# Kernel optimization log

Measured on AMD Instinct MI355X. Metric: run time of the kernel, lower is better.

The kernel has to match this reference:

```python
import jax, jax.numpy as jnp
import numpy as np

RATIO = 0.5


def _fps_indices(points, m):
    """Farthest point sampling indices. points: [B,N,3] -> idx [B,m] (int32).
    Deterministic start at index 0 per batch (torch_geometric fps with a fixed start).
    """
    pts = jax.lax.stop_gradient(points)  # index selection is non-differentiable
    B, N, _ = pts.shape
    idx0 = jnp.zeros((B,), dtype=jnp.int32)
    mind0 = jnp.full((B, N), 1e10, dtype=pts.dtype)  # running min sq-distance to selected set

    def step(carry, _):
        mind, last = carry
        last_pt = jnp.take_along_axis(pts, last[:, None, None], axis=1)  # [B,1,3]
        d = jnp.sum((pts - last_pt) ** 2, axis=-1)                       # [B,N]
        mind = jnp.minimum(mind, d)
        nxt = jnp.argmax(mind, axis=1).astype(jnp.int32)                 # farthest point
        return (mind, nxt), nxt

    _, rest = jax.lax.scan(step, (mind0, idx0), None, length=m - 1)      # [m-1, B]
    return jnp.concatenate([idx0[None, :], rest], axis=0).T              # [B, m]


def setup_inputs() -> dict:
    key = jax.random.key(0)
    k1, k2 = jax.random.split(key)
    points = jax.random.normal(k1, (8, 8192, 3), dtype=jnp.float32)
    features = jax.random.normal(k2, (8, 8192, 256), dtype=jnp.float32)
    return {"points": points, "features": features}


def reference(points, features):
    B, N, _ = points.shape
    m = int(np.ceil(RATIO * N))
    idx = _fps_indices(points, m)                                        # [B, m]
    dp = jnp.take_along_axis(points, idx[:, :, None], axis=1)            # [B, m, 3]
    df = jnp.take_along_axis(features, idx[:, :, None], axis=1)          # [B, m, C]
    return dp, df
```

## Files before the change

kernel.cpp:

```cpp
#include <hip/hip_runtime.h>


typedef float v2f __attribute__((ext_vector_type(2)));

#define BATCH 8
#define NPTS  8192
#define MSEL  4096
#define NFEAT 256
#define BLOCK 1024
#define NWAVE (BLOCK / 64)

__device__ __forceinline__ double sqd(double x) {
    double r;
    asm("v_mul_f64 %0, %1, %1" : "=v"(r) : "v"(x));
    return r;
}

__device__ __forceinline__ unsigned wave_umax_rl(unsigned v) {
    unsigned s;
    asm volatile(
        "s_nop 1\n\t"
        "v_max_u32_dpp %1, %1, %1 row_shr:1  row_mask:0xf bank_mask:0xf bound_ctrl:0\n\t"
        "s_nop 1\n\t"
        "v_max_u32_dpp %1, %1, %1 row_shr:2  row_mask:0xf bank_mask:0xf bound_ctrl:0\n\t"
        "s_nop 1\n\t"
        "v_max_u32_dpp %1, %1, %1 row_shr:4  row_mask:0xf bank_mask:0xf bound_ctrl:0\n\t"
        "s_nop 1\n\t"
        "v_max_u32_dpp %1, %1, %1 row_shr:8  row_mask:0xf bank_mask:0xf bound_ctrl:0\n\t"
        "s_nop 1\n\t"
        "v_max_u32_dpp %1, %1, %1 row_bcast:15 row_mask:0xf bank_mask:0xf bound_ctrl:0\n\t"
        "s_nop 1\n\t"
        "v_max_u32_dpp %1, %1, %1 row_bcast:31 row_mask:0xf bank_mask:0xf bound_ctrl:0\n\t"
        "s_nop 1\n\t"
        "v_readlane_b32 %0, %1, 63"
        : "=s"(s), "+v"(v));
    return s;
}

__launch_bounds__(BLOCK, 1)
__global__ void fps_kernel(const float* __restrict__ pts,
                           float* __restrict__ dp,
                           int* __restrict__ idx_out)
{
    __shared__ float s_pts[NPTS * 3];
    __shared__ unsigned long long s_bmax[2];
    __shared__ int s_widx[2];

    const int b    = blockIdx.x;
    const int tid  = threadIdx.x;
    const int lane = tid & 63;
    const float* p = pts + (size_t)b * NPTS * 3;

    for (int i = tid; i < NPTS * 3; i += BLOCK) s_pts[i] = p[i];
    if (tid == 0) {
        s_bmax[0] = 0ull;        s_bmax[1] = 0ull;
        s_widx[0] = 0x7fffffff;  s_widx[1] = 0x7fffffff;
    }

#define DECLP(P, J0, J1) \
    v2f pxp##P = { p[(tid + J0 * 1024) * 3 + 0], p[(tid + J1 * 1024) * 3 + 0] }; \
    v2f pyp##P = { p[(tid + J0 * 1024) * 3 + 1], p[(tid + J1 * 1024) * 3 + 1] }; \
    v2f pzp##P = { p[(tid + J0 * 1024) * 3 + 2], p[(tid + J1 * 1024) * 3 + 2] };
    DECLP(0, 0, 1) DECLP(1, 2, 3) DECLP(2, 4, 5) DECLP(3, 6, 7)
#undef DECLP
    double mind0 = 1e10, mind1 = 1e10, mind2 = 1e10, mind3 = 1e10;
    double mind4 = 1e10, mind5 = 1e10, mind6 = 1e10, mind7 = 1e10;
    float  mfm0 = 1.0001e10f, mfm1 = 1.0001e10f, mfm2 = 1.0001e10f, mfm3 = 1.0001e10f;
    float  mfm4 = 1.0001e10f, mfm5 = 1.0001e10f, mfm6 = 1.0001e10f, mfm7 = 1.0001e10f;

    float cx = p[0], cy = p[1], cz = p[2];
    if (tid == 0) {
        dp[(size_t)b * MSEL * 3 + 0] = cx;
        dp[(size_t)b * MSEL * 3 + 1] = cy;
        dp[(size_t)b * MSEL * 3 + 2] = cz;
        idx_out[b * MSEL + 0] = 0;
    }

    double   tbv   = 0.0;
    bool     dirty = true;
    unsigned whi = 0u, wlo = 0u;
    unsigned wn  = 0x7fffffffu;

    __syncthreads();

    for (int k = 1; k < MSEL; ++k) {
        const v2f cx2 = {cx, cx}, cy2 = {cy, cy}, cz2 = {cz, cz};

#define EX64(PX, PY, PZ, J) { \
        const double ddx = (double)(PX) - (double)cx; \
        const double ddy = (double)(PY) - (double)cy; \
        const double ddz = (double)(PZ) - (double)cz; \
        const double dd  = (sqd(ddx) + sqd(ddy)) + sqd(ddz); \
        if (dd < mind##J) { mind##J = dd; mfm##J = (float)dd * 1.0001f; dirty = true; } }
#define UPDP(P, J0, J1) { \
        const v2f dx = pxp##P - cx2, dy = pyp##P - cy2, dz = pzp##P - cz2; \
        const v2f d  = dx * dx + dy * dy + dz * dz; \
        if (d.x < mfm##J0) EX64(pxp##P.x, pyp##P.x, pzp##P.x, J0) \
        if (d.y < mfm##J1) EX64(pxp##P.y, pyp##P.y, pzp##P.y, J1) }
        UPDP(0, 0, 1) UPDP(1, 2, 3) UPDP(2, 4, 5) UPDP(3, 6, 7)
#undef UPDP
#undef EX64

        if (__any(dirty)) {
            const double a0 = fmax(mind0, mind1), a1 = fmax(mind2, mind3);
            const double a2 = fmax(mind4, mind5), a3 = fmax(mind6, mind7);
            tbv = fmax(fmax(a0, a1), fmax(a2, a3));
            dirty = false;

            const unsigned long long tb = (unsigned long long)__double_as_longlong(tbv);
            const unsigned thi = (unsigned)(tb >> 32);
            const unsigned tlo = (unsigned)tb;
            whi = wave_umax_rl(thi);
            wlo = wave_umax_rl(thi == whi ? tlo : 0u);

            int n = 0x7fffffff;
            if (thi == whi && tlo == wlo) {
                if (mind7 == tbv) n = tid + 7 * 1024;
                if (mind6 == tbv) n = tid + 6 * 1024;
                if (mind5 == tbv) n = tid + 5 * 1024;
                if (mind4 == tbv) n = tid + 4 * 1024;
                if (mind3 == tbv) n = tid + 3 * 1024;
                if (mind2 == tbv) n = tid + 2 * 1024;
                if (mind1 == tbv) n = tid + 1 * 1024;
                if (mind0 == tbv) n = tid;
            }
            wn = ~wave_umax_rl(~(unsigned)n);
        }

        const unsigned long long mybits =
            ((unsigned long long)whi << 32) | (unsigned long long)wlo;
        if (lane == 0) atomicMax(&s_bmax[k & 1], mybits);
        __syncthreads();

        const unsigned long long bmaxbits = s_bmax[k & 1];
        if (tid == 0) {
            s_bmax[(k + 1) & 1] = 0ull;
            s_widx[(k + 1) & 1] = 0x7fffffff;
        }

        if (lane == 0 && mybits == bmaxbits)
            atomicMin(&s_widx[k & 1], (int)wn);
        __syncthreads();

        const int   widx = s_widx[k & 1];
        const float wx = s_pts[widx * 3 + 0];
        const float wy = s_pts[widx * 3 + 1];
        const float wz = s_pts[widx * 3 + 2];
        if (tid == 0) {
            idx_out[b * MSEL + k] = widx;
            float* o = dp + ((size_t)b * MSEL + k) * 3;
            o[0] = wx; o[1] = wy; o[2] = wz;
        }
        cx = wx; cy = wy; cz = wz;
    }
}

__global__ void gather_kernel(const float* __restrict__ feats,
                              const int* __restrict__ idx,
                              float* __restrict__ df)
{
    const int row  = blockIdx.x * 4 + (threadIdx.x >> 6);
    const int lane = threadIdx.x & 63;
    const int b    = row >> 12;
    const int src  = idx[row];
    const float4* s = (const float4*)(feats + ((size_t)b * NPTS + src) * NFEAT);
    float4*       d = (float4*)(df + (size_t)row * NFEAT);
    d[lane] = s[lane];
}

extern "C" void kernel_launch(void* const* d_in, const int* in_sizes, int n_in,
                              void* d_out, int out_size, void* d_ws, size_t ws_size,
                              hipStream_t stream)
{
    const float* points   = (const float*)d_in[0];
    const float* features = (const float*)d_in[1];
    float* out = (float*)d_out;
    float* dp  = out;
    float* df  = out + (size_t)BATCH * MSEL * 3;
    int*   idx_ws = (int*)d_ws;

    fps_kernel<<<BATCH, BLOCK, 0, stream>>>(points, dp, idx_ws);
    gather_kernel<<<(BATCH * MSEL) / 4, 256, 0, stream>>>(features, idx_ws, df);
}
```

Before: 4.198 ms.

## Morton-sort points and skip FPS updates for threads whose cluster is provably unaffected

Adds a per-batch counting sort of points by a coarse 3D Morton code so each thread owns 8 spatially nearby points. Each thread computes a bounding sphere, and each FPS iteration skips the distance update when the new center is provably farther than the thread's current max min-distance. Tie-breaking packs the original index alongside the sorted position so the lowest original index still wins. The goal is to cut per-iteration ALU and FP64 work, at the cost of an extra sort kernel, extra workspace, and reliance on conservative bound margins for exactness.

```diff
diff --git a/kernel.cpp b/kernel.cpp
--- a/kernel.cpp
+++ b/kernel.cpp
@@ -37,8 +37,80 @@
     return s;
 }
 
+
+__device__ __forceinline__ unsigned part3_4(unsigned v) {
+    return (v & 1u) | ((v & 2u) << 2) | ((v & 4u) << 4) | ((v & 8u) << 6);
+}
+
+__device__ __forceinline__ unsigned mcode(float x, float y, float z) {
+    int qx = (int)((x + 4.f) * 2.f); qx = qx < 0 ? 0 : (qx > 15 ? 15 : qx);
+    int qy = (int)((y + 4.f) * 2.f); qy = qy < 0 ? 0 : (qy > 15 ? 15 : qy);
+    int qz = (int)((z + 4.f) * 2.f); qz = qz < 0 ? 0 : (qz > 15 ? 15 : qz);
+    return part3_4((unsigned)qx) | (part3_4((unsigned)qy) << 1)
+         | (part3_4((unsigned)qz) << 2);
+}
+
+__launch_bounds__(BLOCK, 1)
+__global__ void sort_kernel(const float* __restrict__ pts,
+                            float* __restrict__ spts,
+                            unsigned short* __restrict__ soidx)
+{
+    __shared__ unsigned s_hist[4096];
+    __shared__ unsigned s_part[64];
+    const int b = blockIdx.x, tid = threadIdx.x;
+    const float* p = pts + (size_t)b * NPTS * 3;
+    float* sp = spts + (size_t)b * NPTS * 3;
+    unsigned short* so = soidx + (size_t)b * NPTS;
+
+    for (int i = tid; i < 4096; i += BLOCK) s_hist[i] = 0u;
+    __syncthreads();
+
+    unsigned code[8];
+#pragma unroll
+    for (int j = 0; j < 8; ++j) {
+        const int i = tid * 8 + j;
+        code[j] = mcode(p[i * 3 + 0], p[i * 3 + 1], p[i * 3 + 2]);
+        atomicAdd(&s_hist[code[j]], 1u);
+    }
+    __syncthreads();
+
+    if (tid < 64) {
+        unsigned a = 0;
+        for (int k = 0; k < 64; ++k) a += s_hist[tid * 64 + k];
+        s_part[tid] = a;
+    }
+    __syncthreads();
+    if (tid == 0) {
+        unsigned acc = 0;
+        for (int i = 0; i < 64; ++i) { unsigned c = s_part[i]; s_part[i] = acc; acc += c; }
+    }
+    __syncthreads();
+    if (tid < 64) {
+        unsigned a = s_part[tid];
+        for (int k = 0; k < 64; ++k) {
+            unsigned c = s_hist[tid * 64 + k];
+            s_hist[tid * 64 + k] = a;
+            a += c;
+        }
+    }
+    __syncthreads();
+
+#pragma unroll
+    for (int j = 0; j < 8; ++j) {
+        const int i = tid * 8 + j;
+        const unsigned pos = atomicAdd(&s_hist[code[j]], 1u);
+        sp[pos * 3 + 0] = p[i * 3 + 0];
+        sp[pos * 3 + 1] = p[i * 3 + 1];
+        sp[pos * 3 + 2] = p[i * 3 + 2];
+        so[pos] = (unsigned short)i;
+    }
+}
+
+
 __launch_bounds__(BLOCK, 1)
 __global__ void fps_kernel(const float* __restrict__ pts,
+                           const float* __restrict__ spts,
+                           const unsigned short* __restrict__ soidx,
                            float* __restrict__ dp,
                            int* __restrict__ idx_out)
 {
@@ -49,20 +121,39 @@
     const int b    = blockIdx.x;
     const int tid  = threadIdx.x;
     const int lane = tid & 63;
-    const float* p = pts + (size_t)b * NPTS * 3;
-
-    for (int i = tid; i < NPTS * 3; i += BLOCK) s_pts[i] = p[i];
+    const float* p  = pts  + (size_t)b * NPTS * 3;
+    const float* sp = spts + (size_t)b * NPTS * 3;
+    const unsigned short* so = soidx + (size_t)b * NPTS;
+
+    for (int i = tid; i < NPTS * 3; i += BLOCK) s_pts[i] = sp[i];
     if (tid == 0) {
         s_bmax[0] = 0ull;        s_bmax[1] = 0ull;
         s_widx[0] = 0x7fffffff;  s_widx[1] = 0x7fffffff;
     }
 
-#define DECLP(P, J0, J1) \
-    v2f pxp##P = { p[(tid + J0 * 1024) * 3 + 0], p[(tid + J1 * 1024) * 3 + 0] }; \
-    v2f pyp##P = { p[(tid + J0 * 1024) * 3 + 1], p[(tid + J1 * 1024) * 3 + 1] }; \
-    v2f pzp##P = { p[(tid + J0 * 1024) * 3 + 2], p[(tid + J1 * 1024) * 3 + 2] };
-    DECLP(0, 0, 1) DECLP(1, 2, 3) DECLP(2, 4, 5) DECLP(3, 6, 7)
-#undef DECLP
+    const int base = ((tid >> 6) << 9) + ((tid & 63) << 3);
+    const float4* pb = (const float4*)(sp + (size_t)base * 3);
+    const float4 f0 = pb[0], f1 = pb[1], f2 = pb[2], f3 = pb[3], f4 = pb[4], f5 = pb[5];
+    const v2f pxp0 = {f0.x, f0.w}, pyp0 = {f0.y, f1.x}, pzp0 = {f0.z, f1.y};
+    const v2f pxp1 = {f1.z, f2.y}, pyp1 = {f1.w, f2.z}, pzp1 = {f2.x, f2.w};
+    const v2f pxp2 = {f3.x, f3.w}, pyp2 = {f3.y, f4.x}, pzp2 = {f3.z, f4.y};
+    const v2f pxp3 = {f4.z, f5.y}, pyp3 = {f4.w, f5.z}, pzp3 = {f5.x, f5.w};
+    const uint4 ov = *(const uint4*)(so + base);
+
+    const float tcx = (f0.x + f0.w + f1.z + f2.y + f3.x + f3.w + f4.z + f5.y) * 0.125f;
+    const float tcy = (f0.y + f1.x + f1.w + f2.z + f3.y + f4.x + f4.w + f5.z) * 0.125f;
+    const float tcz = (f0.z + f1.y + f2.x + f2.w + f3.z + f4.y + f5.x + f5.w) * 0.125f;
+    float r2m = 0.f;
+#define RAD(PX, PY, PZ) { \
+        const float rx = (PX) - tcx, ry = (PY) - tcy, rz = (PZ) - tcz; \
+        r2m = fmaxf(r2m, rx * rx + ry * ry + rz * rz); }
+    RAD(pxp0.x, pyp0.x, pzp0.x) RAD(pxp0.y, pyp0.y, pzp0.y)
+    RAD(pxp1.x, pyp1.x, pzp1.x) RAD(pxp1.y, pyp1.y, pzp1.y)
+    RAD(pxp2.x, pyp2.x, pzp2.x) RAD(pxp2.y, pyp2.y, pzp2.y)
+    RAD(pxp3.x, pyp3.x, pzp3.x) RAD(pxp3.y, pyp3.y, pzp3.y)
+#undef RAD
+    const float r_infl = sqrtf(r2m) * 1.00002f + 1e-20f;
+
     double mind0 = 1e10, mind1 = 1e10, mind2 = 1e10, mind3 = 1e10;
     double mind4 = 1e10, mind5 = 1e10, mind6 = 1e10, mind7 = 1e10;
     float  mfm0 = 1.0001e10f, mfm1 = 1.0001e10f, mfm2 = 1.0001e10f, mfm3 = 1.0001e10f;
@@ -76,7 +167,7 @@
         idx_out[b * MSEL + 0] = 0;
     }
 
-    double   tbv   = 0.0;
+    double   tbv   = 1e300;
     bool     dirty = true;
     unsigned whi = 0u, wlo = 0u;
     unsigned wn  = 0x7fffffffu;
@@ -84,47 +175,58 @@
     __syncthreads();
 
     for (int k = 1; k < MSEL; ++k) {
-        const v2f cx2 = {cx, cx}, cy2 = {cy, cy}, cz2 = {cz, cz};
-
+        bool need;
+        {
+            const float ddx = cx - tcx, ddy = cy - tcy, ddz = cz - tcz;
+            const float dist2 = ddx * ddx + ddy * ddy + ddz * ddz;
+            const double sd = (double)(sqrtf(dist2) * 0.99998f) - (double)r_infl;
+            need = !(sd > 0.0 && sd * sd > tbv * 1.000001);
+        }
+
+        if (__any(need)) {
+            if (need) {
+                const v2f cx2 = {cx, cx}, cy2 = {cy, cy}, cz2 = {cz, cz};
 #define EX64(PX, PY, PZ, J) { \
-        const double ddx = (double)(PX) - (double)cx; \
-        const double ddy = (double)(PY) - (double)cy; \
-        const double ddz = (double)(PZ) - (double)cz; \
-        const double dd  = (sqd(ddx) + sqd(ddy)) + sqd(ddz); \
-        if (dd < mind##J) { mind##J = dd; mfm##J = (float)dd * 1.0001f; dirty = true; } }
+                const double ddx = (double)(PX) - (double)cx; \
+                const double ddy = (double)(PY) - (double)cy; \
+                const double ddz = (double)(PZ) - (double)cz; \
+                const double dd  = (sqd(ddx) + sqd(ddy)) + sqd(ddz); \
+                if (dd < mind##J) { mind##J = dd; mfm##J = (float)dd * 1.0001f; dirty = true; } }
 #define UPDP(P, J0, J1) { \
-        const v2f dx = pxp##P - cx2, dy = pyp##P - cy2, dz = pzp##P - cz2; \
-        const v2f d  = dx * dx + dy * dy + dz * dz; \
-        if (d.x < mfm##J0) EX64(pxp##P.x, pyp##P.x, pzp##P.x, J0) \
-        if (d.y < mfm##J1) EX64(pxp##P.y, pyp##P.y, pzp##P.y, J1) }
-        UPDP(0, 0, 1) UPDP(1, 2, 3) UPDP(2, 4, 5) UPDP(3, 6, 7)
+                const v2f dx = pxp##P - cx2, dy = pyp##P - cy2, dz = pzp##P - cz2; \
+                const v2f d  = dx * dx + dy * dy + dz * dz; \
+                if (d.x < mfm##J0) EX64(pxp##P.x, pyp##P.x, pzp##P.x, J0) \
+                if (d.y < mfm##J1) EX64(pxp##P.y, pyp##P.y, pzp##P.y, J1) }
+                UPDP(0, 0, 1) UPDP(1, 2, 3) UPDP(2, 4, 5) UPDP(3, 6, 7)
 #undef UPDP
 #undef EX64
-
-        if (__any(dirty)) {
-            const double a0 = fmax(mind0, mind1), a1 = fmax(mind2, mind3);
-            const double a2 = fmax(mind4, mind5), a3 = fmax(mind6, mind7);
-            tbv = fmax(fmax(a0, a1), fmax(a2, a3));
-            dirty = false;
-
-            const unsigned long long tb = (unsigned long long)__double_as_longlong(tbv);
-            const unsigned thi = (unsigned)(tb >> 32);
-            const unsigned tlo = (unsigned)tb;
-            whi = wave_umax_rl(thi);
-            wlo = wave_umax_rl(thi == whi ? tlo : 0u);
-
-            int n = 0x7fffffff;
-            if (thi == whi && tlo == wlo) {
-                if (mind7 == tbv) n = tid + 7 * 1024;
-                if (mind6 == tbv) n = tid + 6 * 1024;
-                if (mind5 == tbv) n = tid + 5 * 1024;
-                if (mind4 == tbv) n = tid + 4 * 1024;
-                if (mind3 == tbv) n = tid + 3 * 1024;
-                if (mind2 == tbv) n = tid + 2 * 1024;
-                if (mind1 == tbv) n = tid + 1 * 1024;
-                if (mind0 == tbv) n = tid;
             }
-            wn = ~wave_umax_rl(~(unsigned)n);
+
+            if (__any(dirty)) {
+                const double a0 = fmax(mind0, mind1), a1 = fmax(mind2, mind3);
+                const double a2 = fmax(mind4, mind5), a3 = fmax(mind6, mind7);
+                tbv = fmax(fmax(a0, a1), fmax(a2, a3));
+                dirty = false;
+
+                const unsigned long long tb = (unsigned long long)__double_as_longlong(tbv);
+                const unsigned thi = (unsigned)(tb >> 32);
+                const unsigned tlo = (unsigned)tb;
+                whi = wave_umax_rl(thi);
+                wlo = wave_umax_rl(thi == whi ? tlo : 0u);
+
+                unsigned n = 0x7fffffffu;
+                if (thi == whi && tlo == wlo) {
+#define OWN(J, OI) if (mind##J == tbv) { \
+                    const unsigned cand = ((OI) << 13) | (unsigned)(base + J); \
+                    n = cand < n ? cand : n; }
+                    OWN(0, ov.x & 0xffffu) OWN(1, ov.x >> 16)
+                    OWN(2, ov.y & 0xffffu) OWN(3, ov.y >> 16)
+                    OWN(4, ov.z & 0xffffu) OWN(5, ov.z >> 16)
+                    OWN(6, ov.w & 0xffffu) OWN(7, ov.w >> 16)
+#undef OWN
+                }
+                wn = ~wave_umax_rl(~n);
+            }
         }
 
         const unsigned long long mybits =
@@ -142,12 +244,13 @@
             atomicMin(&s_widx[k & 1], (int)wn);
         __syncthreads();
 
-        const int   widx = s_widx[k & 1];
-        const float wx = s_pts[widx * 3 + 0];
-        const float wy = s_pts[widx * 3 + 1];
-        const float wz = s_pts[widx * 3 + 2];
+        const int   wpacked = s_widx[k & 1];
+        const int   wpos  = wpacked & 0x1fff;
+        const float wx = s_pts[wpos * 3 + 0];
+        const float wy = s_pts[wpos * 3 + 1];
+        const float wz = s_pts[wpos * 3 + 2];
         if (tid == 0) {
-            idx_out[b * MSEL + k] = widx;
+            idx_out[b * MSEL + k] = wpacked >> 13;
             float* o = dp + ((size_t)b * MSEL + k) * 3;
             o[0] = wx; o[1] = wy; o[2] = wz;
         }
@@ -177,8 +280,13 @@
     float* out = (float*)d_out;
     float* dp  = out;
     float* df  = out + (size_t)BATCH * MSEL * 3;
+
     int*   idx_ws = (int*)d_ws;
-
-    fps_kernel<<<BATCH, BLOCK, 0, stream>>>(points, dp, idx_ws);
+    float* spts   = (float*)((char*)d_ws + 128 * 1024);
+    unsigned short* soidx =
+        (unsigned short*)((char*)d_ws + 128 * 1024 + BATCH * NPTS * 3 * sizeof(float));
+
+    sort_kernel<<<BATCH, BLOCK, 0, stream>>>(points, spts, soidx);
+    fps_kernel<<<BATCH, BLOCK, 0, stream>>>(points, spts, soidx, dp, idx_ws);
     gather_kernel<<<(BATCH * MSEL) / 4, 256, 0, stream>>>(features, idx_ws, df);
 }
```

New measurement: 5.165 ms. 1.23x slower.

## Carry winner coordinates through shared atomics and batch the per-point distance checks

Applied to the files above, without the earlier changes.

Drops the shared-memory copy of all points. The winning thread now packs its index with each coordinate into 64-bit atomicMin payloads, so the selected point arrives without a dependent LDS lookup and without the per-wave index reduction. The fp32 distance pre-check is also vectorised: all eight thresholds are subtracted at once and a single combined min test guards the fp64 exact path. Costs are three 64-bit LDS atomics per candidate thread and slightly more VALU work in the common no-update case.

```diff
diff --git a/kernel.cpp b/kernel.cpp
--- a/kernel.cpp
+++ b/kernel.cpp
@@ -8,7 +8,6 @@
 #define MSEL  4096
 #define NFEAT 256
 #define BLOCK 1024
-#define NWAVE (BLOCK / 64)
 
 __device__ __forceinline__ double sqd(double x) {
     double r;
@@ -42,19 +41,18 @@
                            float* __restrict__ dp,
                            int* __restrict__ idx_out)
 {
-    __shared__ float s_pts[NPTS * 3];
     __shared__ unsigned long long s_bmax[2];
-    __shared__ int s_widx[2];
+    __shared__ unsigned long long s_pay[2][3];
 
     const int b    = blockIdx.x;
     const int tid  = threadIdx.x;
     const int lane = tid & 63;
     const float* p = pts + (size_t)b * NPTS * 3;
 
-    for (int i = tid; i < NPTS * 3; i += BLOCK) s_pts[i] = p[i];
     if (tid == 0) {
-        s_bmax[0] = 0ull;        s_bmax[1] = 0ull;
-        s_widx[0] = 0x7fffffff;  s_widx[1] = 0x7fffffff;
+        s_bmax[0] = 0ull;  s_bmax[1] = 0ull;
+        s_pay[0][0] = ~0ull; s_pay[0][1] = ~0ull; s_pay[0][2] = ~0ull;
+        s_pay[1][0] = ~0ull; s_pay[1][1] = ~0ull; s_pay[1][2] = ~0ull;
     }
 
 #define DECLP(P, J0, J1) \
@@ -65,8 +63,8 @@
 #undef DECLP
     double mind0 = 1e10, mind1 = 1e10, mind2 = 1e10, mind3 = 1e10;
     double mind4 = 1e10, mind5 = 1e10, mind6 = 1e10, mind7 = 1e10;
-    float  mfm0 = 1.0001e10f, mfm1 = 1.0001e10f, mfm2 = 1.0001e10f, mfm3 = 1.0001e10f;
-    float  mfm4 = 1.0001e10f, mfm5 = 1.0001e10f, mfm6 = 1.0001e10f, mfm7 = 1.0001e10f;
+    v2f mfm01 = {1.0001e10f, 1.0001e10f}, mfm23 = {1.0001e10f, 1.0001e10f};
+    v2f mfm45 = {1.0001e10f, 1.0001e10f}, mfm67 = {1.0001e10f, 1.0001e10f};
 
     float cx = p[0], cy = p[1], cz = p[2];
     if (tid == 0) {
@@ -79,27 +77,44 @@
     double   tbv   = 0.0;
     bool     dirty = true;
     unsigned whi = 0u, wlo = 0u;
-    unsigned wn  = 0x7fffffffu;
+    unsigned nidx = 0xffffffffu;
+    float    nx = 0.f, ny = 0.f, nz = 0.f;
 
     __syncthreads();
 
     for (int k = 1; k < MSEL; ++k) {
         const v2f cx2 = {cx, cx}, cy2 = {cy, cy}, cz2 = {cz, cz};
 
-#define EX64(PX, PY, PZ, J) { \
-        const double ddx = (double)(PX) - (double)cx; \
-        const double ddy = (double)(PY) - (double)cy; \
-        const double ddz = (double)(PZ) - (double)cz; \
-        const double dd  = (sqd(ddx) + sqd(ddy)) + sqd(ddz); \
-        if (dd < mind##J) { mind##J = dd; mfm##J = (float)dd * 1.0001f; dirty = true; } }
-#define UPDP(P, J0, J1) { \
-        const v2f dx = pxp##P - cx2, dy = pyp##P - cy2, dz = pzp##P - cz2; \
-        const v2f d  = dx * dx + dy * dy + dz * dz; \
-        if (d.x < mfm##J0) EX64(pxp##P.x, pyp##P.x, pzp##P.x, J0) \
-        if (d.y < mfm##J1) EX64(pxp##P.y, pyp##P.y, pzp##P.y, J1) }
-        UPDP(0, 0, 1) UPDP(1, 2, 3) UPDP(2, 4, 5) UPDP(3, 6, 7)
-#undef UPDP
+        const v2f dxa = pxp0 - cx2, dya = pyp0 - cy2, dza = pzp0 - cz2;
+        const v2f d0  = dxa * dxa + dya * dya + dza * dza;
+        const v2f dxb = pxp1 - cx2, dyb = pyp1 - cy2, dzb = pzp1 - cz2;
+        const v2f d1  = dxb * dxb + dyb * dyb + dzb * dzb;
+        const v2f dxc = pxp2 - cx2, dyc = pyp2 - cy2, dzc = pzp2 - cz2;
+        const v2f d2  = dxc * dxc + dyc * dyc + dzc * dzc;
+        const v2f dxd = pxp3 - cx2, dyd = pyp3 - cy2, dzd = pzp3 - cz2;
+        const v2f d3  = dxd * dxd + dyd * dyd + dzd * dzd;
+        const v2f t0 = d0 - mfm01, t1 = d1 - mfm23;
+        const v2f t2 = d2 - mfm45, t3 = d3 - mfm67;
+        const float mtx = fminf(fminf(t0.x, t1.x), fminf(t2.x, t3.x));
+        const float mty = fminf(fminf(t0.y, t1.y), fminf(t2.y, t3.y));
+
+        if (mtx < 0.f || mty < 0.f) {
+#define EX64(PX, PY, PZ, MIND, MFE) { \
+            const double ddx = (double)(PX) - (double)cx; \
+            const double ddy = (double)(PY) - (double)cy; \
+            const double ddz = (double)(PZ) - (double)cz; \
+            const double dd  = (sqd(ddx) + sqd(ddy)) + sqd(ddz); \
+            if (dd < MIND) { MIND = dd; MFE = (float)dd * 1.0001f; dirty = true; } }
+            if (t0.x < 0.f) EX64(pxp0.x, pyp0.x, pzp0.x, mind0, mfm01.x)
+            if (t0.y < 0.f) EX64(pxp0.y, pyp0.y, pzp0.y, mind1, mfm01.y)
+            if (t1.x < 0.f) EX64(pxp1.x, pyp1.x, pzp1.x, mind2, mfm23.x)
+            if (t1.y < 0.f) EX64(pxp1.y, pyp1.y, pzp1.y, mind3, mfm23.y)
+            if (t2.x < 0.f) EX64(pxp2.x, pyp2.x, pzp2.x, mind4, mfm45.x)
+            if (t2.y < 0.f) EX64(pxp2.y, pyp2.y, pzp2.y, mind5, mfm45.y)
+            if (t3.x < 0.f) EX64(pxp3.x, pyp3.x, pzp3.x, mind6, mfm67.x)
+            if (t3.y < 0.f) EX64(pxp3.y, pyp3.y, pzp3.y, mind7, mfm67.y)
 #undef EX64
+        }
 
         if (__any(dirty)) {
             const double a0 = fmax(mind0, mind1), a1 = fmax(mind2, mind3);
@@ -113,39 +128,48 @@
             whi = wave_umax_rl(thi);
             wlo = wave_umax_rl(thi == whi ? tlo : 0u);
 
-            int n = 0x7fffffff;
+            nidx = 0xffffffffu;
             if (thi == whi && tlo == wlo) {
-                if (mind7 == tbv) n = tid + 7 * 1024;
-                if (mind6 == tbv) n = tid + 6 * 1024;
-                if (mind5 == tbv) n = tid + 5 * 1024;
-                if (mind4 == tbv) n = tid + 4 * 1024;
-                if (mind3 == tbv) n = tid + 3 * 1024;
-                if (mind2 == tbv) n = tid + 2 * 1024;
-                if (mind1 == tbv) n = tid + 1 * 1024;
-                if (mind0 == tbv) n = tid;
+                if (mind7 == tbv) { nidx = tid + 7*1024; nx = pxp3.y; ny = pyp3.y; nz = pzp3.y; }
+                if (mind6 == tbv) { nidx = tid + 6*1024; nx = pxp3.x; ny = pyp3.x; nz = pzp3.x; }
+                if (mind5 == tbv) { nidx = tid + 5*1024; nx = pxp2.y; ny = pyp2.y; nz = pzp2.y; }
+                if (mind4 == tbv) { nidx = tid + 4*1024; nx = pxp2.x; ny = pyp2.x; nz = pzp2.x; }
+                if (mind3 == tbv) { nidx = tid + 3*1024; nx = pxp1.y; ny = pyp1.y; nz = pzp1.y; }
+                if (mind2 == tbv) { nidx = tid + 2*1024; nx = pxp1.x; ny = pyp1.x; nz = pzp1.x; }
+                if (mind1 == tbv) { nidx = tid + 1*1024; nx = pxp0.y; ny = pyp0.y; nz = pzp0.y; }
+                if (mind0 == tbv) { nidx = tid;          nx = pxp0.x; ny = pyp0.x; nz = pzp0.x; }
             }
-            wn = ~wave_umax_rl(~(unsigned)n);
         }
 
         const unsigned long long mybits =
             ((unsigned long long)whi << 32) | (unsigned long long)wlo;
-        if (lane == 0) atomicMax(&s_bmax[k & 1], mybits);
+        const int buf = k & 1;
+        if (lane == 0) atomicMax(&s_bmax[buf], mybits);
         __syncthreads();
 
-        const unsigned long long bmaxbits = s_bmax[k & 1];
+        const unsigned long long bmaxbits = s_bmax[buf];
         if (tid == 0) {
-            s_bmax[(k + 1) & 1] = 0ull;
-            s_widx[(k + 1) & 1] = 0x7fffffff;
-        }
-
-        if (lane == 0 && mybits == bmaxbits)
-            atomicMin(&s_widx[k & 1], (int)wn);
+            s_bmax[buf ^ 1] = 0ull;
+            s_pay[buf ^ 1][0] = ~0ull;
+            s_pay[buf ^ 1][1] = ~0ull;
+            s_pay[buf ^ 1][2] = ~0ull;
+        }
+
+        if (mybits == bmaxbits && nidx != 0xffffffffu) {
+            const unsigned long long hi = (unsigned long long)nidx << 32;
+            atomicMin(&s_pay[buf][0], hi | (unsigned long long)__float_as_uint(nx));
+            atomicMin(&s_pay[buf][1], hi | (unsigned long long)__float_as_uint(ny));
+            atomicMin(&s_pay[buf][2], hi | (unsigned long long)__float_as_uint(nz));
+        }
         __syncthreads();
 
-        const int   widx = s_widx[k & 1];
-        const float wx = s_pts[widx * 3 + 0];
-        const float wy = s_pts[widx * 3 + 1];
-        const float wz = s_pts[widx * 3 + 2];
+        const unsigned long long p0 = s_pay[buf][0];
+        const unsigned long long p1 = s_pay[buf][1];
+        const unsigned long long p2 = s_pay[buf][2];
+        const int   widx = (int)(p0 >> 32);
+        const float wx = __uint_as_float((unsigned)p0);
+        const float wy = __uint_as_float((unsigned)p1);
+        const float wz = __uint_as_float((unsigned)p2);
         if (tid == 0) {
             idx_out[b * MSEL + k] = widx;
             float* o = dp + ((size_t)b * MSEL + k) * 3;
```

New measurement: 6.141 ms. 1.46x slower.
